# Kernel tuning notes

Measured on AMD Instinct MI355X. Metric: run time of the kernel, lower is better.

The kernel has to match this reference:

```python
import jax, jax.numpy as jnp
import numpy as np


def _ste_round(x):
    # straight-through-estimator round (matches brevitas RoundSte)
    return x + jax.lax.stop_gradient(jnp.round(x) - x)


def _fake_quant(x, bits):
    # symmetric per-tensor fake quantization with max-abs scaling
    qmax = 2.0 ** (bits - 1) - 1.0  # 127 for int8, 7 for int4
    s = jnp.max(jnp.abs(x)) / qmax
    q = jnp.clip(_ste_round(x / s), -qmax, qmax)
    return q * s, s


def setup_inputs() -> dict:
    key = jax.random.key(0)
    k1, k2, k3 = jax.random.split(key, 3)
    B, S, D, H = 8, 2048, 4096, 4096  # tokens = B*S
    x = jax.random.normal(k1, (B * S, D), dtype=jnp.float32)
    W = jax.random.normal(k2, (H, D), dtype=jnp.float32) * (1.0 / np.sqrt(D))
    b = jax.random.normal(k3, (H,), dtype=jnp.float32) * 0.01
    return {"x": x, "W": W, "b": b}


def reference(x, W, b):
    # inputQuant (Int8ActPerTensorFloat) applied twice back-to-back is
    # idempotent in effect; linear1 input_quant re-quantizes the int8 tensor.
    xq, s_in = _fake_quant(x, 8)          # int8 activation quant
    Wq, s_w = _fake_quant(W, 4)           # 4-bit weight quant (weight_bit_width=4)
    s_b = s_in * s_w                      # Int32Bias: scale = input_scale * weight_scale
    bmax = 2.0 ** 31 - 1.0
    bq = jnp.clip(_ste_round(b / s_b), -bmax, bmax) * s_b
    y = xq @ Wq.T + bq                    # quantized matmul (dequantized math)
    yq, _ = _fake_quant(y, 8)             # output_quant Int8ActPerTensorFloat
    return yq
```

## Files before the change

### kernel.cpp

```cpp
#include <hip/hip_runtime.h>
#include <stdint.h>


typedef __attribute__((ext_vector_type(4))) int i32x4;

#define BM 128
#define BN 128
#define BKB 128

__device__ __forceinline__ void async_copy16(const void* g, void* l) {
  __builtin_amdgcn_global_load_lds((const __attribute__((address_space(1))) void*)g,
                                   (__attribute__((address_space(3))) void*)l,
                                   16, 0, 0);
}

__device__ __forceinline__ float wave_max64(float v) {
#pragma unroll
  for (int off = 32; off > 0; off >>= 1) v = fmaxf(v, __shfl_xor(v, off, 64));
  return v;
}

__device__ __forceinline__ float max4(float4 v) {
  return fmaxf(fmaxf(fabsf(v.x), fabsf(v.y)), fmaxf(fabsf(v.z), fabsf(v.w)));
}

#define WBLK 1024
__global__ void maxabs_both(const float4* __restrict__ x, int n4x,
                            const float4* __restrict__ w, int n4w,
                            unsigned* __restrict__ scal) {
  const bool isW = (int)blockIdx.x < WBLK;
  const float4* __restrict__ p = isW ? w : x;
  const int n4 = isW ? n4w : n4x;
  const int bid = isW ? blockIdx.x : blockIdx.x - WBLK;
  const int nb = isW ? WBLK : gridDim.x - WBLK;
  const int stride = nb * blockDim.x;

  float m0 = 0.f, m1 = 0.f, m2 = 0.f, m3 = 0.f;
  int i = bid * blockDim.x + threadIdx.x;
  for (; i + 3 * stride < n4; i += 4 * stride) {
    m0 = fmaxf(m0, max4(p[i]));
    m1 = fmaxf(m1, max4(p[i + stride]));
    m2 = fmaxf(m2, max4(p[i + 2 * stride]));
    m3 = fmaxf(m3, max4(p[i + 3 * stride]));
  }
  for (; i < n4; i += stride) m0 = fmaxf(m0, max4(p[i]));
  float m = wave_max64(fmaxf(fmaxf(m0, m1), fmaxf(m2, m3)));

  __shared__ float wm[4];
  if ((threadIdx.x & 63) == 0) wm[threadIdx.x >> 6] = m;
  __syncthreads();
  if (threadIdx.x == 0)
    atomicMax(&scal[isW ? 1 : 0],
              __float_as_uint(fmaxf(fmaxf(wm[0], wm[1]), fmaxf(wm[2], wm[3]))));
}

__device__ __forceinline__ unsigned pack4(float4 v, float inv, float qmax) {
  unsigned b0 = (unsigned)(int)fminf(fmaxf(rintf(v.x * inv), -qmax), qmax) & 0xffu;
  unsigned b1 = (unsigned)(int)fminf(fmaxf(rintf(v.y * inv), -qmax), qmax) & 0xffu;
  unsigned b2 = (unsigned)(int)fminf(fmaxf(rintf(v.z * inv), -qmax), qmax) & 0xffu;
  unsigned b3 = (unsigned)(int)fminf(fmaxf(rintf(v.w * inv), -qmax), qmax) & 0xffu;
  return b0 | (b1 << 8) | (b2 << 16) | (b3 << 24);
}

__global__ void quant_both(const float4* __restrict__ x, unsigned* __restrict__ xq, int n4x,
                           const float4* __restrict__ w, unsigned* __restrict__ wq, int n4w,
                           const unsigned* __restrict__ scal) {
  const bool isW = (int)blockIdx.x < WBLK;
  const float4* __restrict__ src = isW ? w : x;
  unsigned* __restrict__ dst = isW ? wq : xq;
  const int n4 = isW ? n4w : n4x;
  const int bid = isW ? blockIdx.x : blockIdx.x - WBLK;
  const int nb = isW ? WBLK : gridDim.x - WBLK;
  const float qmax = isW ? 7.f : 127.f;
  const float inv = qmax / __uint_as_float(scal[isW ? 1 : 0]);
  const int stride = nb * blockDim.x;

  int i = bid * blockDim.x + threadIdx.x;
  for (; i + stride < n4; i += 2 * stride) {
    float4 a = src[i];
    float4 b = src[i + stride];
    dst[i] = pack4(a, inv, qmax);
    dst[i + stride] = pack4(b, inv, qmax);
  }
  if (i < n4) dst[i] = pack4(src[i], inv, qmax);
}

__global__ __launch_bounds__(256, 4) void gemm_i8(
    const uint8_t* __restrict__ Aq, const uint8_t* __restrict__ Bq,
    const float* __restrict__ bias, float* __restrict__ Out,
    unsigned* __restrict__ scal, int M, int N, int K) {
  __shared__ uint8_t sA[BM * BKB];
  __shared__ uint8_t sB[BN * BKB];
  __shared__ float wred[4];

  const int t = threadIdx.x;
  const int lane = t & 63, wave = t >> 6;
  const int wm = wave >> 1, wn = wave & 1;
  const int quad = lane >> 4, l16 = lane & 15;
  const int bm = blockIdx.y * BM, bn = blockIdx.x * BN;

  i32x4 acc[4][4] = {};

  for (int k0 = 0; k0 < K; k0 += BKB) {
#pragma unroll
    for (int j = 0; j < 4; ++j) {
      const int id = j * 256 + t;
      const int r = id >> 3;
      const int cc = id & 7;
      const int gc = (cc ^ (r & 7)) << 4;
      async_copy16(Aq + (size_t)(bm + r) * K + k0 + gc, sA + id * 16);
      async_copy16(Bq + (size_t)(bn + r) * K + k0 + gc, sB + id * 16);
    }
    __syncthreads();
#pragma unroll
    for (int kk = 0; kk < 2; ++kk) {
      i32x4 af[4], bf[4];
#pragma unroll
      for (int mt = 0; mt < 4; ++mt) {
        const int row = wm * 64 + mt * 16 + l16;
        const int p = (quad + kk * 4) ^ (row & 7);
        af[mt] = *(const i32x4*)&sA[row * BKB + p * 16];
      }
#pragma unroll
      for (int nt = 0; nt < 4; ++nt) {
        const int row = wn * 64 + nt * 16 + l16;
        const int p = (quad + kk * 4) ^ (row & 7);
        bf[nt] = *(const i32x4*)&sB[row * BKB + p * 16];
      }
#pragma unroll
      for (int mt = 0; mt < 4; ++mt)
#pragma unroll
        for (int nt = 0; nt < 4; ++nt)
          acc[mt][nt] = __builtin_amdgcn_mfma_i32_16x16x64_i8(af[mt], bf[nt], acc[mt][nt], 0, 0, 0);
    }
    __syncthreads();
  }

  const float s_in = __uint_as_float(scal[0]) / 127.0f;
  const float s_w = __uint_as_float(scal[1]) / 7.0f;
  const float s_b = s_in * s_w;
  float bi[4];
#pragma unroll
  for (int nt = 0; nt < 4; ++nt) {
    const int n = bn + wn * 64 + nt * 16 + l16;
    bi[nt] = rintf(bias[n] / s_b);
  }
  float lmax = 0.f;
#pragma unroll
  for (int mt = 0; mt < 4; ++mt) {
#pragma unroll
    for (int r = 0; r < 4; ++r) {
      const int m = bm + wm * 64 + mt * 16 + quad * 4 + r;
      float* orow = Out + (size_t)m * N + bn + wn * 64 + l16;
#pragma unroll
      for (int nt = 0; nt < 4; ++nt) {
        float tv = (float)acc[mt][nt][r] + bi[nt];
        orow[nt * 16] = tv;
        lmax = fmaxf(lmax, fabsf(tv));
      }
    }
  }
  lmax = wave_max64(lmax);
  if (lane == 0) wred[wave] = lmax;
  __syncthreads();
  if (t == 0)
    atomicMax(&scal[2], __float_as_uint(fmaxf(fmaxf(wred[0], wred[1]), fmaxf(wred[2], wred[3]))));
}

__device__ __forceinline__ float4 quantize4(float4 v, float inv, float s_out) {
  v.x = fminf(fmaxf(rintf(v.x * inv), -127.f), 127.f) * s_out;
  v.y = fminf(fmaxf(rintf(v.y * inv), -127.f), 127.f) * s_out;
  v.z = fminf(fmaxf(rintf(v.z * inv), -127.f), 127.f) * s_out;
  v.w = fminf(fmaxf(rintf(v.w * inv), -127.f), 127.f) * s_out;
  return v;
}

__global__ void finalize4(float4* __restrict__ out, int n4, const unsigned* __restrict__ scal) {
  const float s_in = __uint_as_float(scal[0]) / 127.0f;
  const float s_w = __uint_as_float(scal[1]) / 7.0f;
  const float s_b = s_in * s_w;
  const float maxt = __uint_as_float(scal[2]);
  const float s_out = (s_b * maxt) / 127.0f;
  const float inv = 127.0f / maxt;
  const int stride = gridDim.x * blockDim.x;
  int i = blockIdx.x * blockDim.x + threadIdx.x;
  for (; i + stride < n4; i += 2 * stride) {
    float4 a = out[i];
    float4 b = out[i + stride];
    out[i] = quantize4(a, inv, s_out);
    out[i + stride] = quantize4(b, inv, s_out);
  }
  if (i < n4) out[i] = quantize4(out[i], inv, s_out);
}

extern "C" void kernel_launch(void* const* d_in, const int* in_sizes, int n_in,
                              void* d_out, int out_size, void* d_ws, size_t ws_size,
                              hipStream_t stream) {
  const float* x = (const float*)d_in[0];
  const float* W = (const float*)d_in[1];
  const float* b = (const float*)d_in[2];
  float* out = (float*)d_out;

  const int N = in_sizes[2];
  const int K = in_sizes[1] / N;
  const int M = in_sizes[0] / K;

  unsigned* scal = (unsigned*)d_ws;
  const size_t OFF = 4096;
  uint8_t* xq = (uint8_t*)d_ws + OFF;
  uint8_t* wq = xq + (size_t)M * K;

  const int n4x = (M / 4) * K;
  const int n4w = (N / 4) * K;

  hipMemsetAsync(scal, 0, 16, stream);
  maxabs_both<<<WBLK + 4096, 256, 0, stream>>>((const float4*)x, n4x,
                                               (const float4*)W, n4w, scal);
  quant_both<<<WBLK + 4096, 256, 0, stream>>>((const float4*)x, (unsigned*)xq, n4x,
                                              (const float4*)W, (unsigned*)wq, n4w, scal);

  dim3 grid(N / BN, M / BM);
  gemm_i8<<<grid, 256, 0, stream>>>(xq, wq, b, out, scal, M, N, K);

  finalize4<<<8192, 256, 0, stream>>>((float4*)out, (int)((size_t)M * N / 4), scal);
}
```

Before: 876.8 us.

## Double-buffer int8 GEMM with 256x256 tiles, 8 waves and XCD-aware block remap

Grows the GEMM block tile to 256x256 with 512 threads (8 waves, each computing 128x64) and double-buffers the LDS tiles, so the next K-slice is loaded asynchronously while MFMAs run on the current one, gated by vmcnt waits and raw barriers. It also remaps the 1D block index round-robin across the 8 XCDs and raises wave priority around the MFMA bursts. The aim is more data reuse per byte loaded, hidden global-load latency, and better L2 locality. In exchange it uses 128KB of LDS and more accumulator registers, which lowers occupancy, and it adds barriers inside the inner loop.

```diff
diff --git a/kernel.cpp b/kernel.cpp
--- a/kernel.cpp
+++ b/kernel.cpp
@@ -4,8 +4,8 @@
 
 typedef __attribute__((ext_vector_type(4))) int i32x4;
 
-#define BM 128
-#define BN 128
+#define BM 256
+#define BN 256
 #define BKB 128
 
 __device__ __forceinline__ void async_copy16(const void* g, void* l) {
@@ -85,55 +85,93 @@
   if (i < n4) dst[i] = pack4(src[i], inv, qmax);
 }
 
-__global__ __launch_bounds__(256, 4) void gemm_i8(
+__device__ __forceinline__ void stage_tile(const uint8_t* __restrict__ Aq,
+                                           const uint8_t* __restrict__ Bq,
+                                           uint8_t* sa, uint8_t* sb,
+                                           int t, int K, int bm, int bn, int k0) {
+#pragma unroll
+  for (int j = 0; j < 4; ++j) {
+    const int id = j * 512 + t;
+    const int r = id >> 3;
+    const int cc = id & 7;
+    const int gc = (cc ^ (r & 7)) << 4;
+    async_copy16(Aq + (size_t)(bm + r) * K + k0 + gc, sa + id * 16);
+  }
+#pragma unroll
+  for (int j = 0; j < 4; ++j) {
+    const int id = j * 512 + t;
+    const int r = id >> 3;
+    const int cc = id & 7;
+    const int gc = (cc ^ (r & 7)) << 4;
+    async_copy16(Bq + (size_t)(bn + r) * K + k0 + gc, sb + id * 16);
+  }
+}
+
+__global__ __launch_bounds__(512, 2) void gemm_i8(
     const uint8_t* __restrict__ Aq, const uint8_t* __restrict__ Bq,
     const float* __restrict__ bias, float* __restrict__ Out,
     unsigned* __restrict__ scal, int M, int N, int K) {
-  __shared__ uint8_t sA[BM * BKB];
-  __shared__ uint8_t sB[BN * BKB];
-  __shared__ float wred[4];
+  __shared__ uint8_t sA[2][BM * BKB];
+  __shared__ uint8_t sB[2][BN * BKB];
+  __shared__ float wred[8];
 
   const int t = threadIdx.x;
   const int lane = t & 63, wave = t >> 6;
-  const int wm = wave >> 1, wn = wave & 1;
+  const int wm = wave >> 2, wn = wave & 3;
   const int quad = lane >> 4, l16 = lane & 15;
-  const int bm = blockIdx.y * BM, bn = blockIdx.x * BN;
-
-  i32x4 acc[4][4] = {};
-
-  for (int k0 = 0; k0 < K; k0 += BKB) {
-#pragma unroll
-    for (int j = 0; j < 4; ++j) {
-      const int id = j * 256 + t;
-      const int r = id >> 3;
-      const int cc = id & 7;
-      const int gc = (cc ^ (r & 7)) << 4;
-      async_copy16(Aq + (size_t)(bm + r) * K + k0 + gc, sA + id * 16);
-      async_copy16(Bq + (size_t)(bn + r) * K + k0 + gc, sB + id * 16);
+
+  const int nwg = (int)gridDim.x;
+  const int wg = ((int)blockIdx.x & 7) * (nwg >> 3) + ((int)blockIdx.x >> 3);
+  const int nbx = N / BN;
+  const int bm = (wg / nbx) * BM, bn = (wg % nbx) * BN;
+
+  i32x4 acc[8][4] = {};
+  const int NT = K >> 7;
+
+  stage_tile(Aq, Bq, sA[0], sB[0], t, K, bm, bn, 0);
+
+  for (int tt = 0; tt < NT; ++tt) {
+    const int cur = tt & 1;
+    if (tt + 1 < NT) {
+      stage_tile(Aq, Bq, sA[cur ^ 1], sB[cur ^ 1], t, K, bm, bn, (tt + 1) << 7);
+      asm volatile("s_waitcnt vmcnt(8)" ::: "memory");
+    } else {
+      asm volatile("s_waitcnt vmcnt(0)" ::: "memory");
     }
-    __syncthreads();
+    asm volatile("s_barrier" ::: "memory");
+
+    const uint8_t* sa = sA[cur];
+    const uint8_t* sb = sB[cur];
 #pragma unroll
     for (int kk = 0; kk < 2; ++kk) {
-      i32x4 af[4], bf[4];
-#pragma unroll
-      for (int mt = 0; mt < 4; ++mt) {
-        const int row = wm * 64 + mt * 16 + l16;
-        const int p = (quad + kk * 4) ^ (row & 7);
-        af[mt] = *(const i32x4*)&sA[row * BKB + p * 16];
-      }
+      i32x4 bf[4];
 #pragma unroll
       for (int nt = 0; nt < 4; ++nt) {
         const int row = wn * 64 + nt * 16 + l16;
         const int p = (quad + kk * 4) ^ (row & 7);
-        bf[nt] = *(const i32x4*)&sB[row * BKB + p * 16];
+        bf[nt] = *(const i32x4*)&sb[row * BKB + p * 16];
       }
 #pragma unroll
-      for (int mt = 0; mt < 4; ++mt)
-#pragma unroll
-        for (int nt = 0; nt < 4; ++nt)
-          acc[mt][nt] = __builtin_amdgcn_mfma_i32_16x16x64_i8(af[mt], bf[nt], acc[mt][nt], 0, 0, 0);
+      for (int mh = 0; mh < 2; ++mh) {
+        i32x4 af[4];
+#pragma unroll
+        for (int mt = 0; mt < 4; ++mt) {
+          const int row = wm * 128 + mh * 64 + mt * 16 + l16;
+          const int p = (quad + kk * 4) ^ (row & 7);
+          af[mt] = *(const i32x4*)&sa[row * BKB + p * 16];
+        }
+        asm volatile("s_barrier" ::: "memory");
+        __builtin_amdgcn_s_setprio(1);
+#pragma unroll
+        for (int mt = 0; mt < 4; ++mt)
+#pragma unroll
+          for (int nt = 0; nt < 4; ++nt)
+            acc[mh * 4 + mt][nt] = __builtin_amdgcn_mfma_i32_16x16x64_i8(
+                af[mt], bf[nt], acc[mh * 4 + mt][nt], 0, 0, 0);
+        __builtin_amdgcn_s_setprio(0);
+        asm volatile("s_barrier" ::: "memory");
+      }
     }
-    __syncthreads();
   }
 
   const float s_in = __uint_as_float(scal[0]) / 127.0f;
@@ -147,14 +185,14 @@
   }
   float lmax = 0.f;
 #pragma unroll
-  for (int mt = 0; mt < 4; ++mt) {
+  for (int a = 0; a < 8; ++a) {
 #pragma unroll
     for (int r = 0; r < 4; ++r) {
-      const int m = bm + wm * 64 + mt * 16 + quad * 4 + r;
+      const int m = bm + wm * 128 + a * 16 + quad * 4 + r;
       float* orow = Out + (size_t)m * N + bn + wn * 64 + l16;
 #pragma unroll
       for (int nt = 0; nt < 4; ++nt) {
-        float tv = (float)acc[mt][nt][r] + bi[nt];
+        float tv = (float)acc[a][nt][r] + bi[nt];
         orow[nt * 16] = tv;
         lmax = fmaxf(lmax, fabsf(tv));
       }
@@ -163,8 +201,12 @@
   lmax = wave_max64(lmax);
   if (lane == 0) wred[wave] = lmax;
   __syncthreads();
-  if (t == 0)
-    atomicMax(&scal[2], __float_as_uint(fmaxf(fmaxf(wred[0], wred[1]), fmaxf(wred[2], wred[3]))));
+  if (t == 0) {
+    float m = wred[0];
+#pragma unroll
+    for (int i = 1; i < 8; ++i) m = fmaxf(m, wred[i]);
+    atomicMax(&scal[2], __float_as_uint(m));
+  }
 }
 
 __device__ __forceinline__ float4 quantize4(float4 v, float inv, float s_out) {
@@ -219,8 +261,8 @@
   quant_both<<<WBLK + 4096, 256, 0, stream>>>((const float4*)x, (unsigned*)xq, n4x,
                                               (const float4*)W, (unsigned*)wq, n4w, scal);
 
-  dim3 grid(N / BN, M / BM);
-  gemm_i8<<<grid, 256, 0, stream>>>(xq, wq, b, out, scal, M, N, K);
+  const int nblk = (M / BM) * (N / BN);
+  gemm_i8<<<nblk, 512, 0, stream>>>(xq, wq, b, out, scal, M, N, K);
 
   finalize4<<<8192, 256, 0, stream>>>((float4*)out, (int)((size_t)M * N / 4), scal);
 }
```

Measured after the change: 1.003 ms. 14.4% more time.

## Fuse output requantization into persistent GEMM via grid-wide barrier

Applied to the files above, without the earlier changes.

Converts the int8 GEMM into a persistent kernel with a fixed grid that loops over output tiles in an XCD-aware order. After all tiles are written, it uses a global atomic-counter barrier before requantizing each block's own tiles in place, which removes the separate finalize kernel launch. The requantize pass rereads tiles the block just wrote, which may still sit in L2. The grid barrier assumes all 768 blocks are co-resident; with launch bounds lowered to 3 waves per SIMD this needs enough CUs, otherwise it deadlocks. The barrier counter lives in scal[3], which the existing 16-byte memset clears.

```diff
diff --git a/kernel.cpp b/kernel.cpp
--- a/kernel.cpp
+++ b/kernel.cpp
@@ -7,6 +7,7 @@
 #define BM 128
 #define BN 128
 #define BKB 128
+#define GEMM_GRID 768
 
 __device__ __forceinline__ void async_copy16(const void* g, void* l) {
   __builtin_amdgcn_global_load_lds((const __attribute__((address_space(1))) void*)g,
@@ -85,7 +86,15 @@
   if (i < n4) dst[i] = pack4(src[i], inv, qmax);
 }
 
-__global__ __launch_bounds__(256, 4) void gemm_i8(
+__device__ __forceinline__ float4 quantize4(float4 v, float inv, float s_out) {
+  v.x = fminf(fmaxf(rintf(v.x * inv), -127.f), 127.f) * s_out;
+  v.y = fminf(fmaxf(rintf(v.y * inv), -127.f), 127.f) * s_out;
+  v.z = fminf(fmaxf(rintf(v.z * inv), -127.f), 127.f) * s_out;
+  v.w = fminf(fmaxf(rintf(v.w * inv), -127.f), 127.f) * s_out;
+  return v;
+}
+
+__global__ __launch_bounds__(256, 3) void gemm_i8_fused(
     const uint8_t* __restrict__ Aq, const uint8_t* __restrict__ Bq,
     const float* __restrict__ bias, float* __restrict__ Out,
     unsigned* __restrict__ scal, int M, int N, int K) {
@@ -97,100 +106,111 @@
   const int lane = t & 63, wave = t >> 6;
   const int wm = wave >> 1, wn = wave & 1;
   const int quad = lane >> 4, l16 = lane & 15;
-  const int bm = blockIdx.y * BM, bn = blockIdx.x * BN;
-
-  i32x4 acc[4][4] = {};
-
-  for (int k0 = 0; k0 < K; k0 += BKB) {
-#pragma unroll
-    for (int j = 0; j < 4; ++j) {
-      const int id = j * 256 + t;
-      const int r = id >> 3;
-      const int cc = id & 7;
-      const int gc = (cc ^ (r & 7)) << 4;
-      async_copy16(Aq + (size_t)(bm + r) * K + k0 + gc, sA + id * 16);
-      async_copy16(Bq + (size_t)(bn + r) * K + k0 + gc, sB + id * 16);
-    }
-    __syncthreads();
-#pragma unroll
-    for (int kk = 0; kk < 2; ++kk) {
-      i32x4 af[4], bf[4];
-#pragma unroll
-      for (int mt = 0; mt < 4; ++mt) {
-        const int row = wm * 64 + mt * 16 + l16;
-        const int p = (quad + kk * 4) ^ (row & 7);
-        af[mt] = *(const i32x4*)&sA[row * BKB + p * 16];
-      }
-#pragma unroll
-      for (int nt = 0; nt < 4; ++nt) {
-        const int row = wn * 64 + nt * 16 + l16;
-        const int p = (quad + kk * 4) ^ (row & 7);
-        bf[nt] = *(const i32x4*)&sB[row * BKB + p * 16];
-      }
-#pragma unroll
-      for (int mt = 0; mt < 4; ++mt)
-#pragma unroll
-        for (int nt = 0; nt < 4; ++nt)
-          acc[mt][nt] = __builtin_amdgcn_mfma_i32_16x16x64_i8(af[mt], bf[nt], acc[mt][nt], 0, 0, 0);
-    }
-    __syncthreads();
-  }
+
+  const int nbx = N / BN;
+  const int ntiles = (M / BM) * nbx;
+  const int nblk = (int)gridDim.x;
+  const int wg = ((int)blockIdx.x & 7) * (nblk >> 3) + ((int)blockIdx.x >> 3);
 
   const float s_in = __uint_as_float(scal[0]) / 127.0f;
   const float s_w = __uint_as_float(scal[1]) / 7.0f;
   const float s_b = s_in * s_w;
-  float bi[4];
-#pragma unroll
-  for (int nt = 0; nt < 4; ++nt) {
-    const int n = bn + wn * 64 + nt * 16 + l16;
-    bi[nt] = rintf(bias[n] / s_b);
-  }
-  float lmax = 0.f;
-#pragma unroll
-  for (int mt = 0; mt < 4; ++mt) {
-#pragma unroll
-    for (int r = 0; r < 4; ++r) {
-      const int m = bm + wm * 64 + mt * 16 + quad * 4 + r;
-      float* orow = Out + (size_t)m * N + bn + wn * 64 + l16;
-#pragma unroll
-      for (int nt = 0; nt < 4; ++nt) {
-        float tv = (float)acc[mt][nt][r] + bi[nt];
-        orow[nt * 16] = tv;
-        lmax = fmaxf(lmax, fabsf(tv));
+
+  for (int T = wg; T < ntiles; T += nblk) {
+    const int bm = (T / nbx) * BM, bn = (T % nbx) * BN;
+
+    i32x4 acc[4][4] = {};
+    for (int k0 = 0; k0 < K; k0 += BKB) {
+#pragma unroll
+      for (int j = 0; j < 4; ++j) {
+        const int id = j * 256 + t;
+        const int r = id >> 3;
+        const int cc = id & 7;
+        const int gc = (cc ^ (r & 7)) << 4;
+        async_copy16(Aq + (size_t)(bm + r) * K + k0 + gc, sA + id * 16);
+        async_copy16(Bq + (size_t)(bn + r) * K + k0 + gc, sB + id * 16);
       }
-    }
-  }
-  lmax = wave_max64(lmax);
-  if (lane == 0) wred[wave] = lmax;
+      __syncthreads();
+#pragma unroll
+      for (int kk = 0; kk < 2; ++kk) {
+        i32x4 af[4], bf[4];
+#pragma unroll
+        for (int mt = 0; mt < 4; ++mt) {
+          const int row = wm * 64 + mt * 16 + l16;
+          const int p = (quad + kk * 4) ^ (row & 7);
+          af[mt] = *(const i32x4*)&sA[row * BKB + p * 16];
+        }
+#pragma unroll
+        for (int nt = 0; nt < 4; ++nt) {
+          const int row = wn * 64 + nt * 16 + l16;
+          const int p = (quad + kk * 4) ^ (row & 7);
+          bf[nt] = *(const i32x4*)&sB[row * BKB + p * 16];
+        }
+#pragma unroll
+        for (int mt = 0; mt < 4; ++mt)
+#pragma unroll
+          for (int nt = 0; nt < 4; ++nt)
+            acc[mt][nt] = __builtin_amdgcn_mfma_i32_16x16x64_i8(af[mt], bf[nt], acc[mt][nt], 0, 0, 0);
+      }
+      __syncthreads();
+    }
+
+    float bi[4];
+#pragma unroll
+    for (int nt = 0; nt < 4; ++nt) {
+      const int n = bn + wn * 64 + nt * 16 + l16;
+      bi[nt] = rintf(bias[n] / s_b);
+    }
+    float lmax = 0.f;
+#pragma unroll
+    for (int mt = 0; mt < 4; ++mt) {
+#pragma unroll
+      for (int r = 0; r < 4; ++r) {
+        const int m = bm + wm * 64 + mt * 16 + quad * 4 + r;
+        float* orow = Out + (size_t)m * N + bn + wn * 64 + l16;
+#pragma unroll
+        for (int nt = 0; nt < 4; ++nt) {
+          float tv = (float)acc[mt][nt][r] + bi[nt];
+          orow[nt * 16] = tv;
+          lmax = fmaxf(lmax, fabsf(tv));
+        }
+      }
+    }
+    lmax = wave_max64(lmax);
+    if (lane == 0) wred[wave] = lmax;
+    __syncthreads();
+    if (t == 0)
+      atomicMax(&scal[2], __float_as_uint(fmaxf(fmaxf(wred[0], wred[1]), fmaxf(wred[2], wred[3]))));
+    __syncthreads();
+  }
+
+  __threadfence();
+  if (t == 0) {
+    __hip_atomic_fetch_add(&scal[3], 1u, __ATOMIC_RELEASE, __HIP_MEMORY_SCOPE_AGENT);
+    unsigned v;
+    do {
+      __builtin_amdgcn_s_sleep(8);
+      v = __hip_atomic_load(&scal[3], __ATOMIC_ACQUIRE, __HIP_MEMORY_SCOPE_AGENT);
+    } while (v < (unsigned)nblk);
+  }
   __syncthreads();
-  if (t == 0)
-    atomicMax(&scal[2], __float_as_uint(fmaxf(fmaxf(wred[0], wred[1]), fmaxf(wred[2], wred[3]))));
-}
-
-__device__ __forceinline__ float4 quantize4(float4 v, float inv, float s_out) {
-  v.x = fminf(fmaxf(rintf(v.x * inv), -127.f), 127.f) * s_out;
-  v.y = fminf(fmaxf(rintf(v.y * inv), -127.f), 127.f) * s_out;
-  v.z = fminf(fmaxf(rintf(v.z * inv), -127.f), 127.f) * s_out;
-  v.w = fminf(fmaxf(rintf(v.w * inv), -127.f), 127.f) * s_out;
-  return v;
-}
-
-__global__ void finalize4(float4* __restrict__ out, int n4, const unsigned* __restrict__ scal) {
-  const float s_in = __uint_as_float(scal[0]) / 127.0f;
-  const float s_w = __uint_as_float(scal[1]) / 7.0f;
-  const float s_b = s_in * s_w;
-  const float maxt = __uint_as_float(scal[2]);
+
+  const float maxt =
+      __uint_as_float(__hip_atomic_load(&scal[2], __ATOMIC_RELAXED, __HIP_MEMORY_SCOPE_AGENT));
   const float s_out = (s_b * maxt) / 127.0f;
   const float inv = 127.0f / maxt;
-  const int stride = gridDim.x * blockDim.x;
-  int i = blockIdx.x * blockDim.x + threadIdx.x;
-  for (; i + stride < n4; i += 2 * stride) {
-    float4 a = out[i];
-    float4 b = out[i + stride];
-    out[i] = quantize4(a, inv, s_out);
-    out[i + stride] = quantize4(b, inv, s_out);
-  }
-  if (i < n4) out[i] = quantize4(out[i], inv, s_out);
+  const int n4row = N >> 2;
+
+  for (int T = wg; T < ntiles; T += nblk) {
+    const int bm = (T / nbx) * BM, bn = (T % nbx) * BN;
+    float4* tp = (float4*)Out + (size_t)bm * n4row + (bn >> 2) + (t & 31);
+    const int r0 = t >> 5;
+#pragma unroll
+    for (int k = 0; k < 16; ++k) {
+      float4* p = tp + (size_t)(r0 + k * 8) * n4row;
+      *p = quantize4(*p, inv, s_out);
+    }
+  }
 }
 
 extern "C" void kernel_launch(void* const* d_in, const int* in_sizes, int n_in,
@@ -219,8 +239,5 @@
   quant_both<<<WBLK + 4096, 256, 0, stream>>>((const float4*)x, (unsigned*)xq, n4x,
                                               (const float4*)W, (unsigned*)wq, n4w, scal);
 
-  dim3 grid(N / BN, M / BM);
-  gemm_i8<<<grid, 256, 0, stream>>>(xq, wq, b, out, scal, M, N, K);
-
-  finalize4<<<8192, 256, 0, stream>>>((float4*)out, (int)((size_t)M * N / 4), scal);
-}
+  gemm_i8_fused<<<GEMM_GRID, 256, 0, stream>>>(xq, wq, b, out, scal, M, N, K);
+}
```

After: 1.371 ms. 1.56x slower.
